# Optimization experiments

Measured on AMD Instinct MI355X. Metric: run time of the kernel, lower is better.

The kernel has to match this reference:

```python
import jax, jax.numpy as jnp
import numpy as np

NUM_CLASSES = 32  # static stand-in for torch's dynamic max(inputs)+1
B, D, H, W = 4, 256, 256, 256


def setup_inputs() -> dict:
    key = jax.random.key(0)
    k1, k2 = jax.random.split(key)
    inputs = jax.random.randint(k1, (B, D, H, W), 0, NUM_CLASSES, dtype=jnp.int32)
    targets = jax.random.randint(k2, (B, D, H, W), 0, NUM_CLASSES, dtype=jnp.int32)
    smooth = jnp.float32(1.0)
    return {"inputs": inputs, "targets": targets, "smooth": smooth}


def reference(inputs, targets, smooth):
    # Fused one-pass equivalent of the per-class loop:
    #   intersection[b,c] = sum((inputs==c) & (targets==c))  -> bincount of inputs masked where labels agree
    #   total[b,c]        = count(inputs==c) + count(targets==c) -> two bincounts
    b = inputs.shape[0]
    flat_in = inputs.reshape(b, -1)
    flat_tg = targets.reshape(b, -1)

    count = jax.vmap(lambda x: jnp.bincount(x, length=NUM_CLASSES))
    hist_in = count(flat_in).astype(jnp.float32)      # [B, C]
    hist_tg = count(flat_tg).astype(jnp.float32)      # [B, C]

    agree = (flat_in == flat_tg).astype(jnp.float32)  # [B, N]
    inter = jax.vmap(
        lambda x, w: jnp.bincount(x, weights=w, length=NUM_CLASSES)
    )(flat_in, agree)                                  # [B, C]

    total = hist_in + hist_tg
    dice_per_class = 1.0 - (2.0 * inter + smooth) / (total + smooth)  # [B, C]
    dice_loss = dice_per_class.sum(axis=1)            # sum over classes, as the torch loop accumulates
    return dice_loss.mean()
```

## Files before the change

### kernel.cpp

```cpp
#include <hip/hip_runtime.h>

#define NUM_CLASSES 32
#define NBINS (NUM_CLASSES * NUM_CLASSES)

typedef int v4i __attribute__((ext_vector_type(4)));

__global__ void __launch_bounds__(256, 8)
dice_hist_kernel(const int* __restrict__ in,
                 const int* __restrict__ tg,
                 unsigned int* __restrict__ ws,
                 long long nPerB) {
    const int b = blockIdx.y;
    __shared__ unsigned int h[NBINS];
    for (int i = threadIdx.x; i < NBINS; i += blockDim.x) h[i] = 0u;
    __syncthreads();

    const long long base = (long long)b * nPerB;
    const v4i* in4 = (const v4i*)(in + base);
    const v4i* tg4 = (const v4i*)(tg + base);
    const long long n4 = nPerB >> 2;
    const long long stride = (long long)gridDim.x * blockDim.x;

    long long i = (long long)blockIdx.x * blockDim.x + threadIdx.x;

    for (; i + stride < n4; i += 2 * stride) {
        v4i a0 = __builtin_nontemporal_load(&in4[i]);
        v4i t0 = __builtin_nontemporal_load(&tg4[i]);
        v4i a1 = __builtin_nontemporal_load(&in4[i + stride]);
        v4i t1 = __builtin_nontemporal_load(&tg4[i + stride]);
        atomicAdd(&h[((a0.x & 31) << 5) | (t0.x & 31)], 1u);
        atomicAdd(&h[((a0.y & 31) << 5) | (t0.y & 31)], 1u);
        atomicAdd(&h[((a0.z & 31) << 5) | (t0.z & 31)], 1u);
        atomicAdd(&h[((a0.w & 31) << 5) | (t0.w & 31)], 1u);
        atomicAdd(&h[((a1.x & 31) << 5) | (t1.x & 31)], 1u);
        atomicAdd(&h[((a1.y & 31) << 5) | (t1.y & 31)], 1u);
        atomicAdd(&h[((a1.z & 31) << 5) | (t1.z & 31)], 1u);
        atomicAdd(&h[((a1.w & 31) << 5) | (t1.w & 31)], 1u);
    }
    for (; i < n4; i += stride) {
        v4i a = __builtin_nontemporal_load(&in4[i]);
        v4i t = __builtin_nontemporal_load(&tg4[i]);
        atomicAdd(&h[((a.x & 31) << 5) | (t.x & 31)], 1u);
        atomicAdd(&h[((a.y & 31) << 5) | (t.y & 31)], 1u);
        atomicAdd(&h[((a.z & 31) << 5) | (t.z & 31)], 1u);
        atomicAdd(&h[((a.w & 31) << 5) | (t.w & 31)], 1u);
    }
    __syncthreads();

    unsigned int* wsb = ws + b * 96;
    const int t = threadIdx.x;
    if (t < 32) {
        unsigned int s = 0;
        #pragma unroll
        for (int k = 0; k < 32; ++k) s += h[(t << 5) | k];
        atomicAdd(&wsb[t], s);
    } else if (t < 64) {
        const int c = t - 32;
        unsigned int s = 0;
        #pragma unroll
        for (int k = 0; k < 32; ++k) s += h[(k << 5) | c];
        atomicAdd(&wsb[32 + c], s);
    } else if (t < 96) {
        const int c = t - 64;
        atomicAdd(&wsb[64 + c], h[(c << 5) | c]);
    }
}

__global__ void dice_final_kernel(const unsigned int* __restrict__ ws,
                                  const float* __restrict__ smooth_p,
                                  float* __restrict__ out, int B) {
    const double s = (double)smooth_p[0];
    const int lane = threadIdx.x;
    double acc = 0.0;
    for (int idx = lane; idx < B * 32; idx += 64) {
        const int b = idx >> 5, c = idx & 31;
        const unsigned int* wsb = ws + b * 96;
        const double inter = (double)wsb[64 + c];
        const double total = (double)wsb[c] + (double)wsb[32 + c];
        acc += 1.0 - (2.0 * inter + s) / (total + s);
    }
    #pragma unroll
    for (int off = 32; off > 0; off >>= 1) acc += __shfl_down(acc, off);
    if (lane == 0) out[0] = (float)(acc / (double)B);
}

extern "C" void kernel_launch(void* const* d_in, const int* in_sizes, int n_in,
                              void* d_out, int out_size, void* d_ws, size_t ws_size,
                              hipStream_t stream) {
    const int* in = (const int*)d_in[0];
    const int* tg = (const int*)d_in[1];
    const float* smooth = (const float*)d_in[2];
    float* out = (float*)d_out;

    const int B = 4;
    const long long total = (long long)in_sizes[0];
    const long long nPerB = total / B;

    (void)hipMemsetAsync(d_ws, 0, (size_t)(B * 96) * sizeof(unsigned int), stream);

    dim3 grid(512, B);
    dice_hist_kernel<<<grid, dim3(256), 0, stream>>>(in, tg, (unsigned int*)d_ws, nPerB);
    dice_final_kernel<<<1, 64, 0, stream>>>((const unsigned int*)d_ws, smooth, out, B);
}
```

Measured before the change: 96.36 us.

## Fuse final reduction into histogram kernel via last-block counter; unroll loads by four

The separate finalization kernel is removed. Each block increments a global completion counter after flushing its histogram, and the last block to finish computes the dice loss from the workspace. The main loop also now issues four vector loads per input per iteration instead of two, for more memory-level parallelism. This saves one kernel launch at the cost of an extra atomic and fence per block, plus higher register pressure.

```diff
diff --git a/kernel.cpp b/kernel.cpp
--- a/kernel.cpp
+++ b/kernel.cpp
@@ -2,16 +2,21 @@
 
 #define NUM_CLASSES 32
 #define NBINS (NUM_CLASSES * NUM_CLASSES)
+#define B_CONST 4
+#define GRID_X 512
 
 typedef int v4i __attribute__((ext_vector_type(4)));
 
 __global__ void __launch_bounds__(256, 8)
-dice_hist_kernel(const int* __restrict__ in,
-                 const int* __restrict__ tg,
-                 unsigned int* __restrict__ ws,
-                 long long nPerB) {
+dice_fused_kernel(const int* __restrict__ in,
+                  const int* __restrict__ tg,
+                  const float* __restrict__ smooth_p,
+                  unsigned int* __restrict__ ws,
+                  float* __restrict__ out,
+                  long long nPerB, unsigned int gridTotal) {
     const int b = blockIdx.y;
     __shared__ unsigned int h[NBINS];
+    __shared__ bool isLast;
     for (int i = threadIdx.x; i < NBINS; i += blockDim.x) h[i] = 0u;
     __syncthreads();
 
@@ -23,28 +28,32 @@
 
     long long i = (long long)blockIdx.x * blockDim.x + threadIdx.x;
 
-    for (; i + stride < n4; i += 2 * stride) {
+#define ATOM4(a, t)                                      \
+    atomicAdd(&h[((a.x & 31) << 5) | (t.x & 31)], 1u);   \
+    atomicAdd(&h[((a.y & 31) << 5) | (t.y & 31)], 1u);   \
+    atomicAdd(&h[((a.z & 31) << 5) | (t.z & 31)], 1u);   \
+    atomicAdd(&h[((a.w & 31) << 5) | (t.w & 31)], 1u)
+
+    for (; i + 3 * stride < n4; i += 4 * stride) {
         v4i a0 = __builtin_nontemporal_load(&in4[i]);
         v4i t0 = __builtin_nontemporal_load(&tg4[i]);
         v4i a1 = __builtin_nontemporal_load(&in4[i + stride]);
         v4i t1 = __builtin_nontemporal_load(&tg4[i + stride]);
-        atomicAdd(&h[((a0.x & 31) << 5) | (t0.x & 31)], 1u);
-        atomicAdd(&h[((a0.y & 31) << 5) | (t0.y & 31)], 1u);
-        atomicAdd(&h[((a0.z & 31) << 5) | (t0.z & 31)], 1u);
-        atomicAdd(&h[((a0.w & 31) << 5) | (t0.w & 31)], 1u);
-        atomicAdd(&h[((a1.x & 31) << 5) | (t1.x & 31)], 1u);
-        atomicAdd(&h[((a1.y & 31) << 5) | (t1.y & 31)], 1u);
-        atomicAdd(&h[((a1.z & 31) << 5) | (t1.z & 31)], 1u);
-        atomicAdd(&h[((a1.w & 31) << 5) | (t1.w & 31)], 1u);
+        v4i a2 = __builtin_nontemporal_load(&in4[i + 2 * stride]);
+        v4i t2 = __builtin_nontemporal_load(&tg4[i + 2 * stride]);
+        v4i a3 = __builtin_nontemporal_load(&in4[i + 3 * stride]);
+        v4i t3 = __builtin_nontemporal_load(&tg4[i + 3 * stride]);
+        ATOM4(a0, t0);
+        ATOM4(a1, t1);
+        ATOM4(a2, t2);
+        ATOM4(a3, t3);
     }
     for (; i < n4; i += stride) {
         v4i a = __builtin_nontemporal_load(&in4[i]);
         v4i t = __builtin_nontemporal_load(&tg4[i]);
-        atomicAdd(&h[((a.x & 31) << 5) | (t.x & 31)], 1u);
-        atomicAdd(&h[((a.y & 31) << 5) | (t.y & 31)], 1u);
-        atomicAdd(&h[((a.z & 31) << 5) | (t.z & 31)], 1u);
-        atomicAdd(&h[((a.w & 31) << 5) | (t.w & 31)], 1u);
+        ATOM4(a, t);
     }
+#undef ATOM4
     __syncthreads();
 
     unsigned int* wsb = ws + b * 96;
@@ -64,24 +73,33 @@
         const int c = t - 64;
         atomicAdd(&wsb[64 + c], h[(c << 5) | c]);
     }
-}
+    __syncthreads();
 
-__global__ void dice_final_kernel(const unsigned int* __restrict__ ws,
-                                  const float* __restrict__ smooth_p,
-                                  float* __restrict__ out, int B) {
-    const double s = (double)smooth_p[0];
-    const int lane = threadIdx.x;
-    double acc = 0.0;
-    for (int idx = lane; idx < B * 32; idx += 64) {
-        const int b = idx >> 5, c = idx & 31;
-        const unsigned int* wsb = ws + b * 96;
-        const double inter = (double)wsb[64 + c];
-        const double total = (double)wsb[c] + (double)wsb[32 + c];
-        acc += 1.0 - (2.0 * inter + s) / (total + s);
+    if (threadIdx.x == 0) {
+        __threadfence();
+        isLast = (atomicAdd(&ws[B_CONST * 96], 1u) == gridTotal - 1u);
     }
-    #pragma unroll
-    for (int off = 32; off > 0; off >>= 1) acc += __shfl_down(acc, off);
-    if (lane == 0) out[0] = (float)(acc / (double)B);
+    __syncthreads();
+
+    if (isLast && threadIdx.x < 64) {
+        __threadfence();
+        const double s = (double)smooth_p[0];
+        double acc = 0.0;
+        for (int idx = threadIdx.x; idx < B_CONST * 32; idx += 64) {
+            const int bb = idx >> 5, c = idx & 31;
+            const unsigned int* p = ws + bb * 96;
+            const double inter = (double)__hip_atomic_load(
+                &p[64 + c], __ATOMIC_RELAXED, __HIP_MEMORY_SCOPE_AGENT);
+            const double total = (double)__hip_atomic_load(
+                &p[c], __ATOMIC_RELAXED, __HIP_MEMORY_SCOPE_AGENT)
+                               + (double)__hip_atomic_load(
+                &p[32 + c], __ATOMIC_RELAXED, __HIP_MEMORY_SCOPE_AGENT);
+            acc += 1.0 - (2.0 * inter + s) / (total + s);
+        }
+        #pragma unroll
+        for (int off = 32; off > 0; off >>= 1) acc += __shfl_down(acc, off);
+        if (threadIdx.x == 0) out[0] = (float)(acc / (double)B_CONST);
+    }
 }
 
 extern "C" void kernel_launch(void* const* d_in, const int* in_sizes, int n_in,
@@ -92,13 +110,13 @@
     const float* smooth = (const float*)d_in[2];
     float* out = (float*)d_out;
 
-    const int B = 4;
     const long long total = (long long)in_sizes[0];
-    const long long nPerB = total / B;
+    const long long nPerB = total / B_CONST;
 
-    (void)hipMemsetAsync(d_ws, 0, (size_t)(B * 96) * sizeof(unsigned int), stream);
+    (void)hipMemsetAsync(d_ws, 0, (size_t)(B_CONST * 96 + 1) * sizeof(unsigned int), stream);
 
-    dim3 grid(512, B);
-    dice_hist_kernel<<<grid, dim3(256), 0, stream>>>(in, tg, (unsigned int*)d_ws, nPerB);
-    dice_final_kernel<<<1, 64, 0, stream>>>((const unsigned int*)d_ws, smooth, out, B);
+    dim3 grid(GRID_X, B_CONST);
+    dice_fused_kernel<<<grid, dim3(256), 0, stream>>>(
+        in, tg, smooth, (unsigned int*)d_ws, out, nPerB,
+        (unsigned int)(GRID_X * B_CONST));
 }
```

Measured after the change: 188.6 us. 1.96x slower.
